# Performance work log

Hardware: AMD Instinct MI355X
Metric: run time of the kernel (lower is better)

The kernel has to match this reference:

```python
import jax, jax.numpy as jnp
import numpy as np

K = 4  # num_neighbors


def setup_inputs() -> dict:
    key = jax.random.key(0)
    kp, kq = jax.random.split(key)
    points = jax.random.normal(kp, (50000, 3), dtype=jnp.float32)
    queries = jax.random.normal(kq, (4000, 3), dtype=jnp.float32)
    return {"points": points, "queries": queries}


def reference(points, queries):
    # Pairwise Euclidean distances, [M, N] (matches torch.cdist p=2)
    q2 = jnp.sum(queries * queries, axis=-1, keepdims=True)        # [M, 1]
    p2 = jnp.sum(points * points, axis=-1)[None, :]                 # [1, N]
    d2 = q2 + p2 - 2.0 * (queries @ points.T)                       # [M, N]
    dist = jnp.sqrt(jnp.maximum(d2, 0.0))
    # k nearest neighbors: smallest distances
    neg_topk, idx = jax.lax.top_k(-dist, K)                          # [M, K]
    return -neg_topk, idx
```

## Files before the change

kernel.cpp:

```cpp
#include <hip/hip_runtime.h>
#include <math.h>
#include <limits.h>

#define NPTS    50000
#define NCHUNK  16
#define CHUNK   3328
#define NGROUP  13
#define NPAD    (NCHUNK * CHUNK)
#define NQ      4000
#define KNN     4
#define QG      8
#define NWAVE   8000
#define NBLK    (NWAVE / 4)
#define CAP     12
#define BIGF    3.0e38f

#define PK_OFF  0
#define CNT_OFF (NPAD * 16)
#define IL_OFF  (CNT_OFF + NQ * NCHUNK * 4)
#define WS_NEED (IL_OFF + NQ * NCHUNK * CAP * 2)

__device__ __forceinline__ void lex_insert(float (&bd)[KNN], int (&bi)[KNN],
                                           float dist, int idx) {
    if (dist < bd[KNN - 1] || (dist == bd[KNN - 1] && idx < bi[KNN - 1])) {
        bd[KNN - 1] = dist; bi[KNN - 1] = idx;
#pragma unroll
        for (int k = KNN - 1; k > 0; --k) {
            bool sw = (bd[k] < bd[k - 1]) || (bd[k] == bd[k - 1] && bi[k] < bi[k - 1]);
            if (sw) {
                float td = bd[k]; bd[k] = bd[k - 1]; bd[k - 1] = td;
                int   ti = bi[k]; bi[k] = bi[k - 1]; bi[k - 1] = ti;
            }
        }
    }
}

__device__ __forceinline__ void wave_merge4(float (&bd)[KNN], int (&bi)[KNN]) {
    for (int m = 1; m < 64; m <<= 1) {
        float od[KNN]; int oi[KNN];
#pragma unroll
        for (int j = 0; j < KNN; ++j) {
            od[j] = __shfl_xor(bd[j], m, 64);
            oi[j] = __shfl_xor(bi[j], m, 64);
        }
        float md[KNN]; int mi[KNN]; int a = 0, b = 0;
#pragma unroll
        for (int j = 0; j < KNN; ++j) {
            const bool takeA = (bd[a] < od[b]) || (bd[a] == od[b] && bi[a] <= oi[b]);
            if (takeA) { md[j] = bd[a]; mi[j] = bi[a]; ++a; }
            else       { md[j] = od[b]; mi[j] = oi[b]; ++b; }
        }
#pragma unroll
        for (int j = 0; j < KNN; ++j) { bd[j] = md[j]; bi[j] = mi[j]; }
    }
}

__global__ __launch_bounds__(256) void pack_kernel(const float* __restrict__ pts,
                                                   float4* __restrict__ packed) {
    int t = blockIdx.x * 256 + threadIdx.x;
    if (t < NPTS) {
        float x = pts[3 * t], y = pts[3 * t + 1], z = pts[3 * t + 2];
        float s = __fadd_rn(__fadd_rn(__fmul_rn(x, x), __fmul_rn(y, y)),
                            __fmul_rn(z, z));
        packed[t] = make_float4(x, y, z, s);
    } else {
        packed[t] = make_float4(0.f, 0.f, 0.f, BIGF);
    }
}

__device__ __forceinline__ float d2f(float mx, float my, float mz, float qs, float4 P) {
    float t = fmaf(mx, P.x, qs);
    t = fmaf(my, P.y, t);
    t = fmaf(mz, P.z, t);
    return t + P.w;
}

__global__ __launch_bounds__(256) void knn_main(const float4* __restrict__ pk,
                                                const float* __restrict__ queries,
                                                int* __restrict__ cnt,
                                                unsigned short* __restrict__ il) {
    const int lane  = threadIdx.x & 63;
    const int widx  = threadIdx.x >> 6;
    const int chunk = blockIdx.x & 15;
    const int qg    = (blockIdx.x >> 4) * 4 + widx;
    const int qbase = qg * QG;

    float mx[QG], my[QG], mz[QG], qs[QG];
#pragma unroll
    for (int j = 0; j < QG; ++j) {
        float a = queries[(qbase + j) * 3 + 0];
        float b = queries[(qbase + j) * 3 + 1];
        float c = queries[(qbase + j) * 3 + 2];
        mx[j] = __fmul_rn(-2.f, a);
        my[j] = __fmul_rn(-2.f, b);
        mz[j] = __fmul_rn(-2.f, c);
        qs[j] = __fadd_rn(__fadd_rn(__fmul_rn(a, a), __fmul_rn(b, b)),
                          __fmul_rn(c, c));
    }

    const float4* p = pk + chunk * CHUNK + lane;
    float mn[QG];
#pragma unroll
    for (int j = 0; j < QG; ++j) mn[j] = BIGF;

#pragma unroll 1
    for (int g = 0; g < NGROUP; ++g) {
        float4 a = p[0], b = p[64], c = p[128], d = p[192];
        p += 256;
#pragma unroll
        for (int j = 0; j < QG; ++j) {
            float da = d2f(mx[j], my[j], mz[j], qs[j], a);
            float db = d2f(mx[j], my[j], mz[j], qs[j], b);
            float dc = d2f(mx[j], my[j], mz[j], qs[j], c);
            float dd = d2f(mx[j], my[j], mz[j], qs[j], d);
            mn[j] = fminf(mn[j], fminf(fminf(da, db), fminf(dc, dd)));
        }
    }

    float tau2[QG];
#pragma unroll
    for (int j = 0; j < QG; ++j) {
        float v = mn[j], tau = mn[j];
#pragma unroll
        for (int r = 0; r < 4; ++r) {
            float t = v;
#pragma unroll
            for (int s = 1; s < 64; s <<= 1) t = fminf(t, __shfl_xor(t, s, 64));
            tau = t;
            v = (v == t) ? BIGF : v;
        }
        tau2[j] = fmaf(tau, 1.00001f, 1e-4f);
    }

    p = pk + chunk * CHUNK + lane;
    int pb = chunk * CHUNK + lane;
#pragma unroll 1
    for (int g = 0; g < NGROUP; ++g) {
        float4 a = p[0], b = p[64], c = p[128], d = p[192];
        p += 256;
#pragma unroll
        for (int j = 0; j < QG; ++j) {
            float da = d2f(mx[j], my[j], mz[j], qs[j], a);
            float db = d2f(mx[j], my[j], mz[j], qs[j], b);
            float dc = d2f(mx[j], my[j], mz[j], qs[j], c);
            float dd = d2f(mx[j], my[j], mz[j], qs[j], d);
            float t4 = fminf(fminf(da, db), fminf(dc, dd));
            if (t4 <= tau2[j]) {
                const int pool = (qbase + j) * NCHUNK + chunk;
                if (da <= tau2[j]) { int pos = atomicAdd(&cnt[pool], 1); if (pos >= 0 && pos < CAP) il[pool*CAP+pos] = (unsigned short)pb; }
                if (db <= tau2[j]) { int pos = atomicAdd(&cnt[pool], 1); if (pos >= 0 && pos < CAP) il[pool*CAP+pos] = (unsigned short)(pb + 64); }
                if (dc <= tau2[j]) { int pos = atomicAdd(&cnt[pool], 1); if (pos >= 0 && pos < CAP) il[pool*CAP+pos] = (unsigned short)(pb + 128); }
                if (dd <= tau2[j]) { int pos = atomicAdd(&cnt[pool], 1); if (pos >= 0 && pos < CAP) il[pool*CAP+pos] = (unsigned short)(pb + 192); }
            }
        }
        pb += 256;
    }
}

__global__ __launch_bounds__(256) void knn_final(const int* __restrict__ cnt,
                                                 const unsigned short* __restrict__ il,
                                                 const float* __restrict__ points,
                                                 const float* __restrict__ queries,
                                                 float* __restrict__ out) {
    const int q    = blockIdx.x * 4 + (threadIdx.x >> 6);
    const int lane = threadIdx.x & 63;

    const float q0 = queries[q*3+0], q1 = queries[q*3+1], q2v = queries[q*3+2];
    const float q2s = __fadd_rn(__fadd_rn(__fmul_rn(q0,q0), __fmul_rn(q1,q1)),
                                __fmul_rn(q2v,q2v));

    float bd[KNN]; int bi[KNN];
#pragma unroll
    for (int k = 0; k < KNN; ++k) { bd[k] = INFINITY; bi[k] = INT_MAX; }

    int sc[3], sj[3], sn[3];
    bool o = false;
#pragma unroll
    for (int t = 0; t < 3; ++t) {
        int s = lane + t * 64;
        int c = s / CAP;
        sc[t] = c; sj[t] = s - c * CAP;
        sn[t] = cnt[q * NCHUNK + c];
        o = o || (sn[t] > CAP);
    }

    if (!__any(o)) {
#pragma unroll
        for (int t = 0; t < 3; ++t) {
            if (sj[t] < sn[t]) {
                int idx = (int)il[(q * NCHUNK + sc[t]) * CAP + sj[t]];
                float x = points[idx*3], y = points[idx*3+1], z = points[idx*3+2];
                float p2s = __fadd_rn(__fadd_rn(__fmul_rn(x,x), __fmul_rn(y,y)), __fmul_rn(z,z));
                float dot = __fadd_rn(__fadd_rn(__fmul_rn(q0,x), __fmul_rn(q1,y)), __fmul_rn(q2v,z));
                float d2  = __fsub_rn(__fadd_rn(q2s, p2s), __fmul_rn(2.0f, dot));
                lex_insert(bd, bi, __fsqrt_rn(fmaxf(d2, 0.f)), idx);
            }
        }
    } else {
        for (int p = lane; p < NPTS; p += 64) {
            float x = points[p*3], y = points[p*3+1], z = points[p*3+2];
            float p2s = __fadd_rn(__fadd_rn(__fmul_rn(x,x), __fmul_rn(y,y)), __fmul_rn(z,z));
            float dot = __fadd_rn(__fadd_rn(__fmul_rn(q0,x), __fmul_rn(q1,y)), __fmul_rn(q2v,z));
            float d2  = __fsub_rn(__fadd_rn(q2s, p2s), __fmul_rn(2.0f, dot));
            lex_insert(bd, bi, __fsqrt_rn(fmaxf(d2, 0.f)), p);
        }
    }

    wave_merge4(bd, bi);

    if (lane == 0) {
#pragma unroll
        for (int k = 0; k < KNN; ++k) {
            out[q * KNN + k]            = bd[k];
            out[NQ * KNN + q * KNN + k] = (float)bi[k];
        }
    }
}

__global__ __launch_bounds__(256) void knn_fallback(const float* __restrict__ points,
                                                    const float* __restrict__ queries,
                                                    float* __restrict__ out) {
    const int gtid = blockIdx.x * blockDim.x + threadIdx.x;
    const int wave = gtid >> 6;
    const int lane = threadIdx.x & 63;
    if (wave >= NQ) return;
    const float q0 = queries[wave*3+0], q1 = queries[wave*3+1], q2v = queries[wave*3+2];
    const float q2s = __fadd_rn(__fadd_rn(__fmul_rn(q0,q0), __fmul_rn(q1,q1)), __fmul_rn(q2v,q2v));
    float bd[KNN]; int bi[KNN];
#pragma unroll
    for (int j = 0; j < KNN; ++j) { bd[j] = INFINITY; bi[j] = INT_MAX; }
    for (int p = lane; p < NPTS; p += 64) {
        float x = points[p*3], y = points[p*3+1], z = points[p*3+2];
        float p2s = __fadd_rn(__fadd_rn(__fmul_rn(x,x), __fmul_rn(y,y)), __fmul_rn(z,z));
        float dot = __fadd_rn(__fadd_rn(__fmul_rn(q0,x), __fmul_rn(q1,y)), __fmul_rn(q2v,z));
        float d2 = __fsub_rn(__fadd_rn(q2s, p2s), __fmul_rn(2.0f, dot));
        lex_insert(bd, bi, __fsqrt_rn(fmaxf(d2, 0.f)), p);
    }
    wave_merge4(bd, bi);
    if (lane == 0) {
#pragma unroll
        for (int j = 0; j < KNN; ++j) {
            out[wave*KNN+j] = bd[j];
            out[NQ*KNN + wave*KNN + j] = (float)bi[j];
        }
    }
}

extern "C" void kernel_launch(void* const* d_in, const int* in_sizes, int n_in,
                              void* d_out, int out_size, void* d_ws, size_t ws_size,
                              hipStream_t stream) {
    const float* points  = (const float*)d_in[0];
    const float* queries = (const float*)d_in[1];
    float* out = (float*)d_out;

    if (ws_size < (size_t)WS_NEED) {
        knn_fallback<<<(NQ * 64 + 255) / 256, 256, 0, stream>>>(points, queries, out);
        return;
    }

    char* ws = (char*)d_ws;
    float4*         packed = (float4*)(ws + PK_OFF);
    int*            cnt    = (int*)(ws + CNT_OFF);
    unsigned short* il     = (unsigned short*)(ws + IL_OFF);

    pack_kernel<<<NPAD / 256, 256, 0, stream>>>(points, packed);
    (void)hipMemsetAsync(cnt, 0, NQ * NCHUNK * sizeof(int), stream);
    knn_main<<<NBLK, 256, 0, stream>>>(packed, queries, cnt, il);
    knn_final<<<NQ / 4, 256, 0, stream>>>(cnt, il, points, queries, out);
}
```

Before: 98.66 us.

## Pack point pairs SoA-style to use packed FP32 FMA in distance loops

Changes the packed point layout so each pair of points is stored as two float4s (x0,x1,y0,y1 / z0,z1,s0,s1), letting the distance computation use 2-wide vector FMA and min (packed FP32 math on CDNA). This is meant to roughly halve the VALU instruction count in both scan passes of the main kernel. Candidate indices are remapped to the new pair layout, and the final kernel reads original points by index, so correctness depends on that mapping. It risks the compiler not emitting packed instructions and costs some extra shuffling of operands.

```diff
diff --git a/kernel.cpp b/kernel.cpp
--- a/kernel.cpp
+++ b/kernel.cpp
@@ -5,8 +5,10 @@
 #define NPTS    50000
 #define NCHUNK  16
 #define CHUNK   3328
+#define CBUN    1664
 #define NGROUP  13
 #define NPAD    (NCHUNK * CHUNK)
+#define NBUN    (NPAD / 2)
 #define NQ      4000
 #define KNN     4
 #define QG      8
@@ -20,6 +22,8 @@
 #define IL_OFF  (CNT_OFF + NQ * NCHUNK * 4)
 #define WS_NEED (IL_OFF + NQ * NCHUNK * CAP * 2)
 
+typedef float v2f __attribute__((ext_vector_type(2)));
+
 __device__ __forceinline__ void lex_insert(float (&bd)[KNN], int (&bi)[KNN],
                                            float dist, int idx) {
     if (dist < bd[KNN - 1] || (dist == bd[KNN - 1] && idx < bi[KNN - 1])) {
@@ -58,24 +62,31 @@
 __global__ __launch_bounds__(256) void pack_kernel(const float* __restrict__ pts,
                                                    float4* __restrict__ packed) {
     int t = blockIdx.x * 256 + threadIdx.x;
-    if (t < NPTS) {
-        float x = pts[3 * t], y = pts[3 * t + 1], z = pts[3 * t + 2];
-        float s = __fadd_rn(__fadd_rn(__fmul_rn(x, x), __fmul_rn(y, y)),
-                            __fmul_rn(z, z));
-        packed[t] = make_float4(x, y, z, s);
-    } else {
-        packed[t] = make_float4(0.f, 0.f, 0.f, BIGF);
-    }
-}
-
-__device__ __forceinline__ float d2f(float mx, float my, float mz, float qs, float4 P) {
-    float t = fmaf(mx, P.x, qs);
-    t = fmaf(my, P.y, t);
-    t = fmaf(mz, P.z, t);
-    return t + P.w;
-}
-
-__global__ __launch_bounds__(256) void knn_main(const float4* __restrict__ pk,
+    int p0 = 2 * t, p1 = 2 * t + 1;
+    float x0 = 0.f, y0 = 0.f, z0 = 0.f, s0 = BIGF;
+    float x1 = 0.f, y1 = 0.f, z1 = 0.f, s1 = BIGF;
+    if (p0 < NPTS) {
+        x0 = pts[3*p0]; y0 = pts[3*p0+1]; z0 = pts[3*p0+2];
+        s0 = __fadd_rn(__fadd_rn(__fmul_rn(x0,x0), __fmul_rn(y0,y0)), __fmul_rn(z0,z0));
+    }
+    if (p1 < NPTS) {
+        x1 = pts[3*p1]; y1 = pts[3*p1+1]; z1 = pts[3*p1+2];
+        s1 = __fadd_rn(__fadd_rn(__fmul_rn(x1,x1), __fmul_rn(y1,y1)), __fmul_rn(z1,z1));
+    }
+    packed[2*t]     = make_float4(x0, x1, y0, y1);
+    packed[2*t + 1] = make_float4(z0, z1, s0, s1);
+}
+
+__device__ __forceinline__ v2f d2pk(float mx, float my, float mz, float qs,
+                                    float4 XY, float4 ZS) {
+    v2f x = {XY.x, XY.y}, y = {XY.z, XY.w}, z = {ZS.x, ZS.y}, s = {ZS.z, ZS.w};
+    v2f t = __builtin_elementwise_fma((v2f){mx, mx}, x, (v2f){qs, qs});
+    t = __builtin_elementwise_fma((v2f){my, my}, y, t);
+    t = __builtin_elementwise_fma((v2f){mz, mz}, z, t);
+    return t + s;
+}
+
+__global__ __launch_bounds__(256) void knn_main(const float4* __restrict__ pk4,
                                                 const float* __restrict__ queries,
                                                 int* __restrict__ cnt,
                                                 unsigned short* __restrict__ il) {
@@ -98,29 +109,28 @@
                           __fmul_rn(c, c));
     }
 
-    const float4* p = pk + chunk * CHUNK + lane;
-    float mn[QG];
-#pragma unroll
-    for (int j = 0; j < QG; ++j) mn[j] = BIGF;
+    const float4* p = pk4 + 2 * (chunk * CBUN + lane);
+    v2f mn[QG];
+#pragma unroll
+    for (int j = 0; j < QG; ++j) mn[j] = (v2f){BIGF, BIGF};
 
 #pragma unroll 1
     for (int g = 0; g < NGROUP; ++g) {
-        float4 a = p[0], b = p[64], c = p[128], d = p[192];
+        float4 A1 = p[0], A2 = p[1], B1 = p[128], B2 = p[129];
         p += 256;
 #pragma unroll
         for (int j = 0; j < QG; ++j) {
-            float da = d2f(mx[j], my[j], mz[j], qs[j], a);
-            float db = d2f(mx[j], my[j], mz[j], qs[j], b);
-            float dc = d2f(mx[j], my[j], mz[j], qs[j], c);
-            float dd = d2f(mx[j], my[j], mz[j], qs[j], d);
-            mn[j] = fminf(mn[j], fminf(fminf(da, db), fminf(dc, dd)));
+            v2f ta = d2pk(mx[j], my[j], mz[j], qs[j], A1, A2);
+            v2f tb = d2pk(mx[j], my[j], mz[j], qs[j], B1, B2);
+            mn[j] = __builtin_elementwise_min(mn[j],
+                        __builtin_elementwise_min(ta, tb));
         }
     }
 
     float tau2[QG];
 #pragma unroll
     for (int j = 0; j < QG; ++j) {
-        float v = mn[j], tau = mn[j];
+        float v = fminf(mn[j].x, mn[j].y), tau = v;
 #pragma unroll
         for (int r = 0; r < 4; ++r) {
             float t = v;
@@ -132,25 +142,24 @@
         tau2[j] = fmaf(tau, 1.00001f, 1e-4f);
     }
 
-    p = pk + chunk * CHUNK + lane;
-    int pb = chunk * CHUNK + lane;
+    p = pk4 + 2 * (chunk * CBUN + lane);
+    int pb = 2 * (chunk * CBUN + lane);
 #pragma unroll 1
     for (int g = 0; g < NGROUP; ++g) {
-        float4 a = p[0], b = p[64], c = p[128], d = p[192];
+        float4 A1 = p[0], A2 = p[1], B1 = p[128], B2 = p[129];
         p += 256;
 #pragma unroll
         for (int j = 0; j < QG; ++j) {
-            float da = d2f(mx[j], my[j], mz[j], qs[j], a);
-            float db = d2f(mx[j], my[j], mz[j], qs[j], b);
-            float dc = d2f(mx[j], my[j], mz[j], qs[j], c);
-            float dd = d2f(mx[j], my[j], mz[j], qs[j], d);
-            float t4 = fminf(fminf(da, db), fminf(dc, dd));
-            if (t4 <= tau2[j]) {
+            v2f ta = d2pk(mx[j], my[j], mz[j], qs[j], A1, A2);
+            v2f tb = d2pk(mx[j], my[j], mz[j], qs[j], B1, B2);
+            v2f m2 = __builtin_elementwise_min(ta, tb);
+            float m1 = fminf(m2.x, m2.y);
+            if (m1 <= tau2[j]) {
                 const int pool = (qbase + j) * NCHUNK + chunk;
-                if (da <= tau2[j]) { int pos = atomicAdd(&cnt[pool], 1); if (pos >= 0 && pos < CAP) il[pool*CAP+pos] = (unsigned short)pb; }
-                if (db <= tau2[j]) { int pos = atomicAdd(&cnt[pool], 1); if (pos >= 0 && pos < CAP) il[pool*CAP+pos] = (unsigned short)(pb + 64); }
-                if (dc <= tau2[j]) { int pos = atomicAdd(&cnt[pool], 1); if (pos >= 0 && pos < CAP) il[pool*CAP+pos] = (unsigned short)(pb + 128); }
-                if (dd <= tau2[j]) { int pos = atomicAdd(&cnt[pool], 1); if (pos >= 0 && pos < CAP) il[pool*CAP+pos] = (unsigned short)(pb + 192); }
+                if (ta.x <= tau2[j]) { int pos = atomicAdd(&cnt[pool], 1); if (pos >= 0 && pos < CAP) il[pool*CAP+pos] = (unsigned short)pb; }
+                if (ta.y <= tau2[j]) { int pos = atomicAdd(&cnt[pool], 1); if (pos >= 0 && pos < CAP) il[pool*CAP+pos] = (unsigned short)(pb + 1); }
+                if (tb.x <= tau2[j]) { int pos = atomicAdd(&cnt[pool], 1); if (pos >= 0 && pos < CAP) il[pool*CAP+pos] = (unsigned short)(pb + 128); }
+                if (tb.y <= tau2[j]) { int pos = atomicAdd(&cnt[pool], 1); if (pos >= 0 && pos < CAP) il[pool*CAP+pos] = (unsigned short)(pb + 129); }
             }
         }
         pb += 256;
@@ -263,7 +272,7 @@
     int*            cnt    = (int*)(ws + CNT_OFF);
     unsigned short* il     = (unsigned short*)(ws + IL_OFF);
 
-    pack_kernel<<<NPAD / 256, 256, 0, stream>>>(points, packed);
+    pack_kernel<<<NBUN / 256, 256, 0, stream>>>(points, packed);
     (void)hipMemsetAsync(cnt, 0, NQ * NCHUNK * sizeof(int), stream);
     knn_main<<<NBLK, 256, 0, stream>>>(packed, queries, cnt, il);
     knn_final<<<NQ / 4, 256, 0, stream>>>(cnt, il, points, queries, out);
```

New measurement: 102.2 us. 1.04x slower.
